# Kernel optimization log

Measured on AMD Instinct MI355X. Metric: run time of the kernel, lower is better.

The kernel has to match this reference:

```python
import jax, jax.numpy as jnp
import numpy as np


def _unfold(x, kh, kw):
    # torch.nn.functional.unfold ordering: channel-major, then kernel row, then kernel col
    B, C, H, W = x.shape
    Ho, Wo = H - kh + 1, W - kw + 1
    cols = jnp.stack([x[:, :, i:i + Ho, j:j + Wo]
                      for i in range(kh) for j in range(kw)], axis=2)  # [B,C,kh*kw,Ho,Wo]
    return cols.reshape(B, C * kh * kw, Ho * Wo), Ho, Wo


def _conv_unfold_matmul(x, w, b):
    # preprocessing: unfold -> A [B,L,K], B = w.view(O,-1).T [K,O]
    # matmul -> [B,L,O]; postprocessing: transpose, reshape, add bias
    O = w.shape[0]
    kh, kw = w.shape[2], w.shape[3]
    cols, Ho, Wo = _unfold(x, kh, kw)                      # [B,K,L]
    out = jnp.einsum('bkl,ok->bol', cols, w.reshape(O, -1))  # [B,O,L]
    return out.reshape(x.shape[0], O, Ho, Wo) + b[None, :, None, None]


def setup_inputs() -> dict:
    key = jax.random.key(0)
    ks = jax.random.split(key, 9)
    B = 4096
    x = jax.random.normal(ks[0], (B, 1, 28, 28), dtype=jnp.float32)
    w1 = jax.random.normal(ks[1], (10, 1, 10, 10), dtype=jnp.float32) * 0.1
    b1 = jax.random.normal(ks[2], (10,), dtype=jnp.float32) * 0.1
    w2 = jax.random.normal(ks[3], (20, 10, 10, 10), dtype=jnp.float32) * 0.03
    b2 = jax.random.normal(ks[4], (20,), dtype=jnp.float32) * 0.1
    w3 = jax.random.normal(ks[5], (20, 20, 5, 5), dtype=jnp.float32) * 0.04
    b3 = jax.random.normal(ks[6], (20,), dtype=jnp.float32) * 0.1
    wf = jax.random.normal(ks[7], (10, 720), dtype=jnp.float32) * 0.04
    bf = jax.random.normal(ks[8], (10,), dtype=jnp.float32) * 0.1
    return {"x": x, "w1": w1, "b1": b1, "w2": w2, "b2": b2,
            "w3": w3, "b3": b3, "wf": wf, "bf": bf}


def reference(x, w1, b1, w2, b2, w3, b3, wf, bf):
    h = jax.nn.relu(_conv_unfold_matmul(x, w1, b1))   # [B,10,19,19]
    h = jax.nn.relu(_conv_unfold_matmul(h, w2, b2))   # [B,20,10,10]
    h = jax.nn.relu(_conv_unfold_matmul(h, w3, b3))   # [B,20,6,6]
    h = h.reshape(-1, 720)
    return h @ wf.T + bf                               # [B,10]
```

## Files before the change

kernel.cpp:

```cpp
#include <hip/hip_runtime.h>


typedef short s16x4 __attribute__((ext_vector_type(4)));
typedef short s16x8 __attribute__((ext_vector_type(8)));
typedef float f32x4 __attribute__((ext_vector_type(4)));

#define ROW1 248
#define ROW2 248
#define H1SZ 4712
#define H2SZ 2480
#define XOFF 9424
#define SM_BYTES 22048

static __device__ __forceinline__ unsigned short f2bf(float f) {
    union { float f; unsigned int u; } v; v.f = f;
    unsigned int u = v.u;
    unsigned int r = (u + 0x7fffu + ((u >> 16) & 1u)) >> 16;
    return (unsigned short)r;
}

static __device__ __forceinline__ s16x8 cat8(s16x4 lo, s16x4 hi) {
    return __builtin_shufflevector(lo, hi, 0, 1, 2, 3, 4, 5, 6, 7);
}

__global__ __launch_bounds__(256) void wprep_k(const float* __restrict__ w1,
                                               const float* __restrict__ w2,
                                               const float* __restrict__ w3,
                                               unsigned short* __restrict__ wbuf) {
    int e = blockIdx.x * 256 + threadIdx.x;
    if (e < 40960) {
        int t = e & 7, lane = (e >> 3) & 63, nt = (e >> 9) & 1;
        int ck = (e >> 10) & 3, i = e >> 12;
        int k = ck * 32 + ((lane >> 4) & 3) * 8 + t;
        int o = nt * 16 + (lane & 15);
        int j = k / 12, c = k % 12;
        float val = (j < 10 && c < 10 && o < 20) ? w2[o * 1000 + c * 100 + i * 10 + j] : 0.f;
        wbuf[e] = f2bf(val);
    } else if (e < 61440) {
        int e2 = e - 40960;
        int t = e2 & 7, lane = (e2 >> 3) & 63, nt = (e2 >> 9) & 1;
        int ck = (e2 >> 10) & 3, i = e2 >> 12;
        int k = ck * 32 + ((lane >> 4) & 3) * 8 + t;
        int o = nt * 16 + (lane & 15);
        int j = k / 20, c = k % 20;
        float val = (j < 5 && o < 20) ? w3[o * 500 + c * 25 + i * 5 + j] : 0.f;
        wbuf[e] = f2bf(val);
    } else {
        int e2 = e - 61440;
        int t = e2 & 7, lane = (e2 >> 3) & 63;
        int kc = (e2 >> 9) % 9, nt = (e2 >> 9) / 9;
        int n = nt * 16 + (lane & 15);
        int k = kc * 32 + ((lane >> 4) & 3) * 8 + t;
        float val = 0.f;
        if (n < 190 && k < 280) {
            int ox = n / 10, o = n - ox * 10;
            int i = k / 28, xc = k - i * 28;
            int j = xc - ox;
            if (j >= 0 && j < 10) val = w1[o * 100 + i * 10 + j];
        }
        wbuf[61440 + e2] = f2bf(val);
    }
}

__global__ __launch_bounds__(128, 4) void fused_k(const float* __restrict__ x,
                                                  const float* __restrict__ b1,
                                                  const unsigned short* __restrict__ wbuf2,
                                                  const unsigned short* __restrict__ wbuf3,
                                                  const unsigned short* __restrict__ wband,
                                                  const float* __restrict__ b2,
                                                  const float* __restrict__ b3,
                                                  const float* __restrict__ wf,
                                                  const float* __restrict__ bf,
                                                  float* __restrict__ out) {
    __shared__ __align__(16) unsigned char smem[SM_BYTES];
    unsigned short* sm16 = (unsigned short*)smem;
    unsigned short* h1  = sm16;
    unsigned short* xbf = sm16 + XOFF;

    const int tid = threadIdx.x;
    const int wave = tid >> 6, lane = tid & 63;
    const int b0 = blockIdx.x * 2;
    const int quad = lane >> 4, lm = lane & 15;

    {
        const float4* src = (const float4*)(x + (size_t)b0 * 784);
        for (int k = tid; k < 392; k += 128) {
            float4 v = src[k];
            int img = (k >= 196);
            int idx = k - img * 196;
            s16x4 p = { (short)f2bf(v.x), (short)f2bf(v.y),
                        (short)f2bf(v.z), (short)f2bf(v.w) };
            *(s16x4*)(xbf + img * 800 + idx * 4) = p;
        }
        if (tid < 32) xbf[(tid >> 4) * 800 + 784 + (tid & 15)] = 0;
        for (int e = tid; e < 190; e += 128) {
            int img = (e >= 95); int e2 = e - img * 95;
            int row = e2 / 5, seg = e2 - row * 5;
            *(s16x4*)(h1 + img * H1SZ + row * ROW1 + 228 + seg * 4) = (s16x4){0, 0, 0, 0};
        }
        for (int e = tid; e < 722; e += 128) {
            int img = (e >= 361); int e2 = e - img * 361;
            int oy = e2 / 19, ox = e2 - oy * 19;
            *(unsigned int*)(h1 + img * H1SZ + oy * ROW1 + ox * 12 + 10) = 0u;
        }
    }
    __syncthreads();

    {
        int ab[4];
        {
            int r0 = lm;
            int r1 = lm + 16; if (r1 > 18) r1 = 18;
            ab[0] = r0 * 28 + quad * 8;
            ab[1] = r1 * 28 + quad * 8;
            ab[2] = 800 + r0 * 28 + quad * 8;
            ab[3] = 800 + r1 * 28 + quad * 8;
        }
        const unsigned short* wb = wband + lane * 8;
#pragma unroll
        for (int g = 0; g < 2; ++g) {
            f32x4 acc1[3][4] = {};
#pragma unroll
            for (int kc = 0; kc < 9; ++kc) {
                s16x8 a[4];
#pragma unroll
                for (int mt = 0; mt < 4; ++mt)
                    a[mt] = cat8(*(const s16x4*)(xbf + ab[mt] + kc * 32),
                                 *(const s16x4*)(xbf + ab[mt] + kc * 32 + 4));
#pragma unroll
                for (int q = 0; q < 3; ++q) {
                    int nt = wave * 6 + g * 3 + q;
                    s16x8 bw = *(const s16x8*)(wb + (nt * 9 + kc) * 512);
#pragma unroll
                    for (int mt = 0; mt < 4; ++mt)
                        acc1[q][mt] = __builtin_amdgcn_mfma_f32_16x16x32_bf16(a[mt], bw, acc1[q][mt], 0, 0, 0);
                }
            }
#pragma unroll
            for (int q = 0; q < 3; ++q) {
                int n = (wave * 6 + g * 3 + q) * 16 + lm;
                if (n < 190) {
                    int ox = n / 10, o = n - ox * 10;
                    float bias = b1[o];
#pragma unroll
                    for (int mt = 0; mt < 4; ++mt) {
                        int img = mt >> 1, half = mt & 1;
#pragma unroll
                        for (int r = 0; r < 4; ++r) {
                            int oy = half * 16 + quad * 4 + r;
                            if (oy < 19)
                                h1[img * H1SZ + oy * ROW1 + ox * 12 + o] =
                                    f2bf(fmaxf(acc1[q][mt][r] + bias, 0.f));
                        }
                    }
                }
            }
        }
    }
    __syncthreads();

    const unsigned short* h1w = h1 + wave * H1SZ;
    int abase[7];
#pragma unroll
    for (int mt = 0; mt < 7; ++mt) {
        int m = mt * 16 + lm; if (m > 99) m = 99;
        int y = m / 10, xx = m - 10 * y;
        abase[mt] = y * ROW1 + xx * 12 + quad * 8;
    }
    f32x4 acc[7][2] = {};
    {
        const unsigned short* wptr = wbuf2 + lane * 8;
        s16x8 wc0 = *(const s16x8*)(wptr);
        s16x8 wc1 = *(const s16x8*)(wptr + 512);
#pragma unroll
        for (int it = 0; it < 40; ++it) {
            s16x8 wn0 = *(const s16x8*)(wptr + (it + 1) * 1024);
            s16x8 wn1 = *(const s16x8*)(wptr + (it + 1) * 1024 + 512);
            const unsigned short* sb = h1w + (it >> 2) * ROW1 + (it & 3) * 32;
            s16x8 af[7];
#pragma unroll
            for (int mt = 0; mt < 7; ++mt)
                af[mt] = cat8(*(const s16x4*)(sb + abase[mt]),
                              *(const s16x4*)(sb + abase[mt] + 4));
#pragma unroll
            for (int mt = 0; mt < 7; ++mt) {
                acc[mt][0] = __builtin_amdgcn_mfma_f32_16x16x32_bf16(af[mt], wc0, acc[mt][0], 0, 0, 0);
                acc[mt][1] = __builtin_amdgcn_mfma_f32_16x16x32_bf16(af[mt], wc1, acc[mt][1], 0, 0, 0);
            }
            wc0 = wn0; wc1 = wn1;
        }
    }
    __syncthreads();

    unsigned short* h2w = sm16 + wave * H2SZ;
    for (int e = lane; e < 120; e += 64) {
        int row = e / 12, seg = e - row * 12;
        *(s16x4*)(h2w + row * ROW2 + 200 + seg * 4) = (s16x4){0, 0, 0, 0};
    }
#pragma unroll
    for (int mt = 0; mt < 7; ++mt) {
#pragma unroll
        for (int nt = 0; nt < 2; ++nt) {
            int o = nt * 16 + lm;
            if (o < 20) {
                float bias = b2[o];
#pragma unroll
                for (int r = 0; r < 4; ++r) {
                    int pos = mt * 16 + quad * 4 + r;
                    if (pos < 100) {
                        int y2 = pos / 10, x2 = pos - 10 * y2;
                        h2w[y2 * ROW2 + x2 * 20 + o] =
                            f2bf(fmaxf(acc[mt][nt][r] + bias, 0.f));
                    }
                }
            }
        }
    }

    int abase3[3];
#pragma unroll
    for (int mt = 0; mt < 3; ++mt) {
        int m = mt * 16 + lm; if (m > 35) m = 35;
        int oy = m / 6, ox = m - 6 * oy;
        abase3[mt] = oy * ROW2 + ox * 20 + quad * 8;
    }
    f32x4 acc3[3][2] = {};
    {
        const unsigned short* wptr = wbuf3 + lane * 8;
        s16x8 wc0 = *(const s16x8*)(wptr);
        s16x8 wc1 = *(const s16x8*)(wptr + 512);
#pragma unroll
        for (int it = 0; it < 20; ++it) {
            s16x8 wn0 = *(const s16x8*)(wptr + (it + 1) * 1024);
            s16x8 wn1 = *(const s16x8*)(wptr + (it + 1) * 1024 + 512);
            const unsigned short* sb = h2w + (it >> 2) * ROW2 + (it & 3) * 32;
            s16x8 af[3];
#pragma unroll
            for (int mt = 0; mt < 3; ++mt)
                af[mt] = cat8(*(const s16x4*)(sb + abase3[mt]),
                              *(const s16x4*)(sb + abase3[mt] + 4));
#pragma unroll
            for (int mt = 0; mt < 3; ++mt) {
                acc3[mt][0] = __builtin_amdgcn_mfma_f32_16x16x32_bf16(af[mt], wc0, acc3[mt][0], 0, 0, 0);
                acc3[mt][1] = __builtin_amdgcn_mfma_f32_16x16x32_bf16(af[mt], wc1, acc3[mt][1], 0, 0, 0);
            }
            wc0 = wn0; wc1 = wn1;
        }
    }

    float* h3w = (float*)(smem + wave * (H2SZ * 2));
#pragma unroll
    for (int mt = 0; mt < 3; ++mt) {
#pragma unroll
        for (int nt = 0; nt < 2; ++nt) {
            int o = nt * 16 + lm;
            if (o < 20) {
                float b3v = b3[o];
#pragma unroll
                for (int r = 0; r < 4; ++r) {
                    int pos = mt * 16 + quad * 4 + r;
                    if (pos < 36)
                        h3w[o * 36 + pos] = fmaxf(acc3[mt][nt][r] + b3v, 0.f);
                }
            }
        }
    }

    float part[10];
#pragma unroll
    for (int n = 0; n < 10; ++n) part[n] = 0.f;
#pragma unroll 1
    for (int s = 0; s < 12; ++s) {
        int k = s * 64 + lane;
        if (k < 720) {
            float v = h3w[k];
#pragma unroll
            for (int n = 0; n < 10; ++n)
                part[n] = fmaf(v, wf[n * 720 + k], part[n]);
        }
    }
#pragma unroll
    for (int n = 0; n < 10; ++n) {
#pragma unroll
        for (int off = 32; off >= 1; off >>= 1)
            part[n] += __shfl_xor(part[n], off, 64);
    }
    if (lane == 0) {
        float* dst = out + (size_t)(b0 + wave) * 10;
#pragma unroll
        for (int n = 0; n < 10; ++n) dst[n] = part[n] + bf[n];
    }
}

extern "C" void kernel_launch(void* const* d_in, const int* in_sizes, int n_in,
                              void* d_out, int out_size, void* d_ws, size_t ws_size,
                              hipStream_t stream) {
    (void)n_in; (void)out_size; (void)ws_size;
    const float* x  = (const float*)d_in[0];
    const float* w1 = (const float*)d_in[1];
    const float* b1 = (const float*)d_in[2];
    const float* w2 = (const float*)d_in[3];
    const float* b2 = (const float*)d_in[4];
    const float* w3 = (const float*)d_in[5];
    const float* b3 = (const float*)d_in[6];
    const float* wf = (const float*)d_in[7];
    const float* bf = (const float*)d_in[8];
    float* out = (float*)d_out;

    const int B = in_sizes[0] / 784;

    unsigned short* wbuf = (unsigned short*)d_ws;

    wprep_k<<<456, 256, 0, stream>>>(w1, w2, w3, wbuf);
    fused_k<<<B / 2, 128, 0, stream>>>(x, b1, wbuf, wbuf + 40960, wbuf + 61440,
                                       b2, b3, wf, bf, out);
}
```

Measured before the change: 147.1 us.

## Make each wave own one image end-to-end and drop block barriers

Each wave now processes a single image through all conv stages using its own shared-memory region, so the block-wide __syncthreads between stages are removed and conv1 work is split per image instead of per output-channel tile. The h1 row stride is shrunk and h2/h3 alias the h1 buffer, cutting shared-memory footprint, and padding zeroing is replaced by masking the tail K chunk in registers. MFMA sections are wrapped in s_setprio and the FC loop drops its per-iteration bound check. The risk is that each wave now reloads all conv1 weight tiles itself (double the per-wave weight traffic), and aliasing relies on the intra-wave ordering of LDS accesses.

```diff
diff --git a/kernel.cpp b/kernel.cpp
--- a/kernel.cpp
+++ b/kernel.cpp
@@ -5,12 +5,12 @@
 typedef short s16x8 __attribute__((ext_vector_type(8)));
 typedef float f32x4 __attribute__((ext_vector_type(4)));
 
-#define ROW1 248
+#define ROW1 228
 #define ROW2 248
-#define H1SZ 4712
-#define H2SZ 2480
-#define XOFF 9424
-#define SM_BYTES 22048
+#define H1SZ 4332
+#define IMSZ 5116
+#define SM_ELEMS 10232
+#define XBOFF 4332
 
 static __device__ __forceinline__ unsigned short f2bf(float f) {
     union { float f; unsigned int u; } v; v.f = f;
@@ -72,84 +72,71 @@
                                                   const float* __restrict__ wf,
                                                   const float* __restrict__ bf,
                                                   float* __restrict__ out) {
-    __shared__ __align__(16) unsigned char smem[SM_BYTES];
-    unsigned short* sm16 = (unsigned short*)smem;
-    unsigned short* h1  = sm16;
-    unsigned short* xbf = sm16 + XOFF;
+    __shared__ __align__(16) unsigned short sm16[SM_ELEMS];
 
     const int tid = threadIdx.x;
     const int wave = tid >> 6, lane = tid & 63;
-    const int b0 = blockIdx.x * 2;
+    const int img = blockIdx.x * 2 + wave;
     const int quad = lane >> 4, lm = lane & 15;
 
-    {
-        const float4* src = (const float4*)(x + (size_t)b0 * 784);
-        for (int k = tid; k < 392; k += 128) {
+    unsigned short* h1w  = sm16 + wave * IMSZ;
+    unsigned short* xbfw = h1w + XBOFF;
+
+    {
+        const float4* src = (const float4*)(x + (size_t)img * 784);
+        for (int k = lane; k < 196; k += 64) {
             float4 v = src[k];
-            int img = (k >= 196);
-            int idx = k - img * 196;
             s16x4 p = { (short)f2bf(v.x), (short)f2bf(v.y),
                         (short)f2bf(v.z), (short)f2bf(v.w) };
-            *(s16x4*)(xbf + img * 800 + idx * 4) = p;
-        }
-        if (tid < 32) xbf[(tid >> 4) * 800 + 784 + (tid & 15)] = 0;
-        for (int e = tid; e < 190; e += 128) {
-            int img = (e >= 95); int e2 = e - img * 95;
-            int row = e2 / 5, seg = e2 - row * 5;
-            *(s16x4*)(h1 + img * H1SZ + row * ROW1 + 228 + seg * 4) = (s16x4){0, 0, 0, 0};
-        }
-        for (int e = tid; e < 722; e += 128) {
-            int img = (e >= 361); int e2 = e - img * 361;
-            int oy = e2 / 19, ox = e2 - oy * 19;
-            *(unsigned int*)(h1 + img * H1SZ + oy * ROW1 + ox * 12 + 10) = 0u;
-        }
-    }
-    __syncthreads();
-
-    {
-        int ab[4];
-        {
-            int r0 = lm;
-            int r1 = lm + 16; if (r1 > 18) r1 = 18;
-            ab[0] = r0 * 28 + quad * 8;
-            ab[1] = r1 * 28 + quad * 8;
-            ab[2] = 800 + r0 * 28 + quad * 8;
-            ab[3] = 800 + r1 * 28 + quad * 8;
-        }
+            *(s16x4*)(xbfw + k * 4) = p;
+        }
+        for (int e = lane; e < 361; e += 64) {
+            int oy = e / 19, ox = e - oy * 19;
+            *(unsigned int*)(h1w + oy * ROW1 + ox * 12 + 10) = 0u;
+        }
+    }
+
+    {
+        int ab0 = lm * 28 + quad * 8;
+        int r1 = lm + 16; if (r1 > 18) r1 = 18;
+        int ab1 = r1 * 28 + quad * 8;
         const unsigned short* wb = wband + lane * 8;
 #pragma unroll
         for (int g = 0; g < 2; ++g) {
-            f32x4 acc1[3][4] = {};
+            f32x4 acc1[6][2] = {};
 #pragma unroll
             for (int kc = 0; kc < 9; ++kc) {
-                s16x8 a[4];
-#pragma unroll
-                for (int mt = 0; mt < 4; ++mt)
-                    a[mt] = cat8(*(const s16x4*)(xbf + ab[mt] + kc * 32),
-                                 *(const s16x4*)(xbf + ab[mt] + kc * 32 + 4));
-#pragma unroll
-                for (int q = 0; q < 3; ++q) {
-                    int nt = wave * 6 + g * 3 + q;
+                s16x8 a0, a1;
+                if (kc == 8 && quad == 3) {
+                    a0 = (s16x8){0,0,0,0,0,0,0,0};
+                    a1 = a0;
+                } else {
+                    a0 = cat8(*(const s16x4*)(xbfw + ab0 + kc * 32),
+                              *(const s16x4*)(xbfw + ab0 + kc * 32 + 4));
+                    a1 = cat8(*(const s16x4*)(xbfw + ab1 + kc * 32),
+                              *(const s16x4*)(xbfw + ab1 + kc * 32 + 4));
+                }
+#pragma unroll
+                for (int q = 0; q < 6; ++q) {
+                    int nt = g * 6 + q;
                     s16x8 bw = *(const s16x8*)(wb + (nt * 9 + kc) * 512);
-#pragma unroll
-                    for (int mt = 0; mt < 4; ++mt)
-                        acc1[q][mt] = __builtin_amdgcn_mfma_f32_16x16x32_bf16(a[mt], bw, acc1[q][mt], 0, 0, 0);
-                }
-            }
-#pragma unroll
-            for (int q = 0; q < 3; ++q) {
-                int n = (wave * 6 + g * 3 + q) * 16 + lm;
+                    acc1[q][0] = __builtin_amdgcn_mfma_f32_16x16x32_bf16(a0, bw, acc1[q][0], 0, 0, 0);
+                    acc1[q][1] = __builtin_amdgcn_mfma_f32_16x16x32_bf16(a1, bw, acc1[q][1], 0, 0, 0);
+                }
+            }
+#pragma unroll
+            for (int q = 0; q < 6; ++q) {
+                int n = (g * 6 + q) * 16 + lm;
                 if (n < 190) {
                     int ox = n / 10, o = n - ox * 10;
                     float bias = b1[o];
 #pragma unroll
-                    for (int mt = 0; mt < 4; ++mt) {
-                        int img = mt >> 1, half = mt & 1;
+                    for (int mt = 0; mt < 2; ++mt) {
 #pragma unroll
                         for (int r = 0; r < 4; ++r) {
-                            int oy = half * 16 + quad * 4 + r;
+                            int oy = mt * 16 + quad * 4 + r;
                             if (oy < 19)
-                                h1[img * H1SZ + oy * ROW1 + ox * 12 + o] =
+                                h1w[oy * ROW1 + ox * 12 + o] =
                                     f2bf(fmaxf(acc1[q][mt][r] + bias, 0.f));
                         }
                     }
@@ -157,9 +144,7 @@
             }
         }
     }
-    __syncthreads();
-
-    const unsigned short* h1w = h1 + wave * H1SZ;
+
     int abase[7];
 #pragma unroll
     for (int mt = 0; mt < 7; ++mt) {
@@ -182,21 +167,18 @@
             for (int mt = 0; mt < 7; ++mt)
                 af[mt] = cat8(*(const s16x4*)(sb + abase[mt]),
                               *(const s16x4*)(sb + abase[mt] + 4));
+            __builtin_amdgcn_s_setprio(1);
 #pragma unroll
             for (int mt = 0; mt < 7; ++mt) {
                 acc[mt][0] = __builtin_amdgcn_mfma_f32_16x16x32_bf16(af[mt], wc0, acc[mt][0], 0, 0, 0);
                 acc[mt][1] = __builtin_amdgcn_mfma_f32_16x16x32_bf16(af[mt], wc1, acc[mt][1], 0, 0, 0);
             }
+            __builtin_amdgcn_s_setprio(0);
             wc0 = wn0; wc1 = wn1;
         }
     }
-    __syncthreads();
-
-    unsigned short* h2w = sm16 + wave * H2SZ;
-    for (int e = lane; e < 120; e += 64) {
-        int row = e / 12, seg = e - row * 12;
-        *(s16x4*)(h2w + row * ROW2 + 200 + seg * 4) = (s16x4){0, 0, 0, 0};
-    }
+
+    unsigned short* h2w = h1w;
 #pragma unroll
     for (int mt = 0; mt < 7; ++mt) {
 #pragma unroll
@@ -239,16 +221,18 @@
             for (int mt = 0; mt < 3; ++mt)
                 af[mt] = cat8(*(const s16x4*)(sb + abase3[mt]),
                               *(const s16x4*)(sb + abase3[mt] + 4));
+            __builtin_amdgcn_s_setprio(1);
 #pragma unroll
             for (int mt = 0; mt < 3; ++mt) {
                 acc3[mt][0] = __builtin_amdgcn_mfma_f32_16x16x32_bf16(af[mt], wc0, acc3[mt][0], 0, 0, 0);
                 acc3[mt][1] = __builtin_amdgcn_mfma_f32_16x16x32_bf16(af[mt], wc1, acc3[mt][1], 0, 0, 0);
             }
+            __builtin_amdgcn_s_setprio(0);
             wc0 = wn0; wc1 = wn1;
         }
     }
 
-    float* h3w = (float*)(smem + wave * (H2SZ * 2));
+    float* h3w = (float*)h1w;
 #pragma unroll
     for (int mt = 0; mt < 3; ++mt) {
 #pragma unroll
@@ -269,10 +253,17 @@
     float part[10];
 #pragma unroll
     for (int n = 0; n < 10; ++n) part[n] = 0.f;
-#pragma unroll 1
-    for (int s = 0; s < 12; ++s) {
+#pragma unroll 2
+    for (int s = 0; s < 11; ++s) {
         int k = s * 64 + lane;
-        if (k < 720) {
+        float v = h3w[k];
+#pragma unroll
+        for (int n = 0; n < 10; ++n)
+            part[n] = fmaf(v, wf[n * 720 + k], part[n]);
+    }
+    {
+        int k = 704 + lane;
+        if (lane < 16) {
             float v = h3w[k];
 #pragma unroll
             for (int n = 0; n < 10; ++n)
@@ -286,7 +277,7 @@
             part[n] += __shfl_xor(part[n], off, 64);
     }
     if (lane == 0) {
-        float* dst = out + (size_t)(b0 + wave) * 10;
+        float* dst = out + (size_t)img * 10;
 #pragma unroll
         for (int n = 0; n < 10; ++n) dst[n] = part[n] + bf[n];
     }
```

Result: no change. 145.7 us (-1.0%).
